# Kernel optimization log

Hardware: AMD Instinct MI355X
Metric: run time of the kernel (lower is better)

The kernel has to match this reference:

```python
import jax, jax.numpy as jnp
import numpy as np

N = 50000      # nodes
E = 640000     # edges
HID = 64       # hid_dim (per-head channels C)
HEADS = 4
D = HID * HEADS  # 256, conv output dim (concat=True)
LN_EPS = 1e-5


def setup_inputs() -> dict:
    key = jax.random.key(0)
    ks = jax.random.split(key, 10)
    def w(k, shape, scale=0.05):
        return jax.random.normal(k, shape, dtype=jnp.float32) * scale
    x = jax.random.normal(ks[0], (N, HID), dtype=jnp.float32)
    edge_index = jax.random.randint(ks[1], (2, E), 0, N)
    return {
        'x': x,
        'edge_index': edge_index,
        'Wq': w(ks[2], (D, HID)), 'bq': jnp.zeros((D,), jnp.float32),
        'Wk': w(ks[3], (D, HID)), 'bk': jnp.zeros((D,), jnp.float32),
        'Wv': w(ks[4], (D, HID)), 'bv': jnp.zeros((D,), jnp.float32),
        'Wskip': w(ks[5], (D, HID)), 'bskip': jnp.zeros((D,), jnp.float32),
        'Wbeta': w(ks[6], (1, 3 * D)),
        'ln_g': jnp.ones((D,), jnp.float32), 'ln_b': jnp.zeros((D,), jnp.float32),
        'Wproj': w(ks[7], (HID, D)), 'bproj': jnp.zeros((HID,), jnp.float32),
    }


def _layer(x, edge_index, Wq, bq, Wk, bk, Wv, bv, Wskip, bskip, Wbeta, ln_g, ln_b, Wproj, bproj):
    src, dst = edge_index[0], edge_index[1]  # message flows src -> dst
    # q/k/v projections, [N, H, C]
    q = (x @ Wq.T + bq).reshape(N, HEADS, HID)
    k = (x @ Wk.T + bk).reshape(N, HEADS, HID)
    v = (x @ Wv.T + bv).reshape(N, HEADS, HID)
    # edge-wise attention logits: [E, H]
    alpha = jnp.einsum('ehc,ehc->eh', q[dst], k[src]) / jnp.sqrt(jnp.float32(HID))
    # per-destination-node softmax (segment softmax)
    m = jax.ops.segment_max(alpha, dst, num_segments=N)          # [N, H]
    ex = jnp.exp(alpha - m[dst])                                 # [E, H]
    s = jax.ops.segment_sum(ex, dst, num_segments=N)             # [N, H]
    attn = ex / (s[dst] + 1e-16)                                 # [E, H]
    # weighted scatter-aggregate of values -> [N, H*C]
    msg = (v[src] * attn[..., None]).reshape(E, D)
    out = jax.ops.segment_sum(msg, dst, num_segments=N)          # [N, D]
    # beta gated skip (TransformerConv beta=True, root_weight=True)
    x_r = x @ Wskip.T + bskip                                    # [N, D]
    beta = jax.nn.sigmoid(jnp.concatenate([out, x_r, out - x_r], axis=-1) @ Wbeta.T)  # [N, 1]
    h = beta * x_r + (1.0 - beta) * out
    # LayerNorm over last dim
    mu = jnp.mean(h, axis=-1, keepdims=True)
    var = jnp.var(h, axis=-1, keepdims=True)
    h = (h - mu) * jax.lax.rsqrt(var + LN_EPS) * ln_g + ln_b
    # projection + residual + ReLU (dropout = identity in eval)
    h = h @ Wproj.T + bproj
    return jax.nn.relu(h + x)


def reference(x, edge_index, Wq, bq, Wk, bk, Wv, bv, Wskip, bskip, Wbeta, ln_g, ln_b, Wproj, bproj):
    return _layer(x, edge_index, Wq, bq, Wk, bk, Wv, bv, Wskip, bskip, Wbeta, ln_g, ln_b, Wproj, bproj)
```

## Files before the change

### kernel.cpp

```cpp
#include <hip/hip_runtime.h>
#include <stdint.h>

#define NND 50000
#define NED 640000

typedef unsigned short u16;
typedef unsigned int u32;
typedef __attribute__((ext_vector_type(8))) short short8;
typedef __attribute__((ext_vector_type(4))) float f32x4;
typedef __attribute__((ext_vector_type(2))) float fx2;

__device__ __forceinline__ float bf2f(u16 u) {
    union { u32 i; float f; } x; x.i = ((u32)u) << 16; return x.f;
}
__device__ __forceinline__ u16 f2bf(float f) {
    union { u32 i; float f; } x; x.f = f;
    u32 u = x.i;
    return (u16)((u + 0x7fffu + ((u >> 16) & 1u)) >> 16);
}
__device__ __forceinline__ float bflo(u32 w) {
    union { u32 i; float f; } x; x.i = w << 16; return x.f;
}
__device__ __forceinline__ float bfhi(u32 w) {
    union { u32 i; float f; } x; x.i = w & 0xffff0000u; return x.f;
}
__device__ __forceinline__ u32 pk2(float lo, float hi) {
    return (u32)f2bf(lo) | ((u32)f2bf(hi) << 16);
}
__device__ __forceinline__ u32 pk_fp8_4(u32 w0, u32 w1) {
    u32 p = __builtin_amdgcn_cvt_pk_fp8_f32(bflo(w0), bfhi(w0), 0, false);
    p = __builtin_amdgcn_cvt_pk_fp8_f32(bflo(w1), bfhi(w1), p, true);
    return p;
}
__device__ __forceinline__ void dec8v(u32 a, u32 b, fx2* f) {
    f[0] = __builtin_amdgcn_cvt_pk_f32_fp8(a, false);
    f[1] = __builtin_amdgcn_cvt_pk_f32_fp8(a, true);
    f[2] = __builtin_amdgcn_cvt_pk_f32_fp8(b, false);
    f[3] = __builtin_amdgcn_cvt_pk_f32_fp8(b, true);
}

__global__ void k_wt(const float* __restrict__ Wq, const float* __restrict__ Wk,
                     const float* __restrict__ Wv, const float* __restrict__ Ws,
                     const float* __restrict__ Wp,
                     const float* __restrict__ bq, const float* __restrict__ bk,
                     const float* __restrict__ bv, const float* __restrict__ bs,
                     u16* __restrict__ wb, float* __restrict__ bias_c,
                     u16* __restrict__ wpA) {
    int idx = blockIdx.x * 256 + threadIdx.x;
    if (idx < 65536) {
        int j = idx & 7;
        int lane = (idx >> 3) & 63;
        int q = (idx >> 9) & 1;
        int dt = idx >> 10;
        int dim = dt * 16 + (lane & 15);
        int k = q * 32 + ((lane >> 4) & 3) * 8 + j;
        int mat = dim >> 8, r = dim & 255;
        const float* W = (mat == 0) ? Wq : (mat == 1) ? Wk : (mat == 2) ? Wv : Ws;
        float v = W[r * 64 + k] * ((mat == 0) ? 0.125f : 1.0f);
        wb[idx] = f2bf(v);
    } else if (idx < 65536 + 1024) {
        int dim = idx - 65536;
        int mat = dim >> 8, r = dim & 255;
        const float* B = (mat == 0) ? bq : (mat == 1) ? bk : (mat == 2) ? bv : bs;
        bias_c[dim] = B[r] * ((mat == 0) ? 0.125f : 1.0f);
    } else if (idx < 65536 + 1024 + 16384) {
        int w = idx - 66560;
        int j = w & 7;
        int lane = (w >> 3) & 63;
        int kc = (w >> 9) & 7;
        int mt = w >> 12;
        int dim = mt * 16 + (lane & 15);
        int k = kc * 32 + ((lane >> 4) & 3) * 8 + j;
        wpA[w] = f2bf(Wp[dim * 256 + k]);
    }
}

#define CNT_BLKS 2500
#define PPAD 1040
__global__ __launch_bounds__(256) void k_fillproj(
    const int* __restrict__ esrc, const int* __restrict__ edst,
    int* __restrict__ deg, int* __restrict__ csr,
    const float* __restrict__ x, const u16* __restrict__ wb,
    const float* __restrict__ bias_c,
    uint2* __restrict__ q8, uint4* __restrict__ kv8, u16* __restrict__ xr16)
{
    __shared__ u16 hb[16 * PPAD];
    if (blockIdx.x < CNT_BLKS) {
        int e = blockIdx.x * 256 + threadIdx.x;
        if (e < NED) {
            int d = edst[e];
            int pos = atomicAdd(&deg[d], 1);
            if (pos < 64) csr[(d << 6) + pos] = esrc[e];
        }
        return;
    }
    const int t = threadIdx.x;
    const int wave = t >> 6, lane = t & 63;
    const int node0 = (blockIdx.x - CNT_BLKS) * 16;
    const int lr = lane & 15, quad = lane >> 4;

    int node = node0 + lr;
    if (node > NND - 1) node = NND - 1;
    short8 xf0, xf1;
    {
        const float* xp = x + (size_t)node * 64 + quad * 8;
        float4 a = *reinterpret_cast<const float4*>(xp);
        float4 b = *reinterpret_cast<const float4*>(xp + 4);
        float4 c = *reinterpret_cast<const float4*>(xp + 32);
        float4 d = *reinterpret_cast<const float4*>(xp + 36);
        xf0[0] = (short)f2bf(a.x); xf0[1] = (short)f2bf(a.y);
        xf0[2] = (short)f2bf(a.z); xf0[3] = (short)f2bf(a.w);
        xf0[4] = (short)f2bf(b.x); xf0[5] = (short)f2bf(b.y);
        xf0[6] = (short)f2bf(b.z); xf0[7] = (short)f2bf(b.w);
        xf1[0] = (short)f2bf(c.x); xf1[1] = (short)f2bf(c.y);
        xf1[2] = (short)f2bf(c.z); xf1[3] = (short)f2bf(c.w);
        xf1[4] = (short)f2bf(d.x); xf1[5] = (short)f2bf(d.y);
        xf1[6] = (short)f2bf(d.z); xf1[7] = (short)f2bf(d.w);
    }
    #pragma unroll 4
    for (int dtl = 0; dtl < 16; ++dtl) {
        int dt = wave * 16 + dtl;
        const u16* wp = wb + (size_t)(dt * 2) * 512 + lane * 8;
        short8 a0 = *reinterpret_cast<const short8*>(wp);
        short8 a1 = *reinterpret_cast<const short8*>(wp + 512);
        f32x4 bias = *reinterpret_cast<const f32x4*>(bias_c + dt * 16 + quad * 4);
        f32x4 acc = {0.f, 0.f, 0.f, 0.f};
        acc = __builtin_amdgcn_mfma_f32_16x16x32_bf16(a0, xf0, acc, 0, 0, 0);
        acc = __builtin_amdgcn_mfma_f32_16x16x32_bf16(a1, xf1, acc, 0, 0, 0);
        uint2 st;
        st.x = pk2(acc[0] + bias[0], acc[1] + bias[1]);
        st.y = pk2(acc[2] + bias[2], acc[3] + bias[3]);
        *reinterpret_cast<uint2*>(&hb[lr * PPAD + dt * 16 + quad * 4]) = st;
    }
    __syncthreads();
    #pragma unroll
    for (int it = 0; it < 2; ++it) {
        int idx = it * 256 + t;
        int nip = idx >> 5, g = idx & 31;
        int gnode = node0 + nip;
        if (gnode < NND) {
            const u16* hp = &hb[nip * PPAD];
            *reinterpret_cast<uint4*>(xr16 + (size_t)gnode * 256 + g * 8) =
                *reinterpret_cast<const uint4*>(hp + 768 + g * 8);
            uint4 qw = *reinterpret_cast<const uint4*>(hp + g * 8);
            uint2 qs;
            qs.x = pk_fp8_4(qw.x, qw.y);
            qs.y = pk_fp8_4(qw.z, qw.w);
            q8[(size_t)gnode * 32 + g] = qs;
            uint4 kw = *reinterpret_cast<const uint4*>(hp + 256 + g * 8);
            uint4 vw = *reinterpret_cast<const uint4*>(hp + 512 + g * 8);
            uint4 kvs;
            kvs.x = pk_fp8_4(kw.x, kw.y);
            kvs.y = pk_fp8_4(kw.z, kw.w);
            kvs.z = pk_fp8_4(vw.x, vw.y);
            kvs.w = pk_fp8_4(vw.z, vw.w);
            kv8[(size_t)gnode * 32 + g] = kvs;
        }
    }
}

#define PS 264
__global__ __launch_bounds__(256) void k_attnepi(
    const int* __restrict__ deg, const int* __restrict__ csr,
    const uint2* __restrict__ q8, const uint4* __restrict__ kv8,
    const u16* __restrict__ xr16, const float* __restrict__ x,
    const float* __restrict__ Wbeta, const float* __restrict__ ln_g,
    const float* __restrict__ ln_b, const u16* __restrict__ wpA,
    const float* __restrict__ bproj, float* __restrict__ y)
{
    __shared__ u16 hn[16 * PS];
    const int t = threadIdx.x;
    const int wave = t >> 6, lane = t & 63;
    const int l32 = lane & 31, half = lane >> 5;
    const int lr = lane & 15, grp = lane >> 4;
    const int base = blockIdx.x * 16;

    for (int nt = 0; nt < 4; ++nt) {
        int lid = wave * 4 + nt;
        int node = base + lid;
        if (node >= NND) break;
        uint2 qv = q8[(size_t)node * 32 + l32];
        fx2 q[4];
        dec8v(qv.x, qv.y, q);
        int dg = __builtin_amdgcn_readfirstlane(deg[node]);
        if (dg > 64) dg = 64;
        int r0 = node << 6;
        int r1 = r0 + dg;
        float s = 0.f;
        fx2 acc0 = {0.f, 0.f}, acc1 = {0.f, 0.f}, acc2 = {0.f, 0.f}, acc3 = {0.f, 0.f};
        int i = r0;
        for (; i + 8 <= r1; i += 8) {
            int c0 = csr[i + 0], c1 = csr[i + 1], c2 = csr[i + 2], c3 = csr[i + 3];
            int c4 = csr[i + 4], c5 = csr[i + 5], c6 = csr[i + 6], c7 = csr[i + 7];
            int e0 = half ? c4 : c0;
            int e1 = half ? c5 : c1;
            int e2 = half ? c6 : c2;
            int e3 = half ? c7 : c3;
            uint4 kv0 = kv8[(size_t)e0 * 32 + l32];
            uint4 kv1 = kv8[(size_t)e1 * 32 + l32];
            uint4 kv2 = kv8[(size_t)e2 * 32 + l32];
            uint4 kv3 = kv8[(size_t)e3 * 32 + l32];
            fx2 k0[4], k1[4], k2[4], k3[4];
            dec8v(kv0.x, kv0.y, k0); dec8v(kv1.x, kv1.y, k1);
            dec8v(kv2.x, kv2.y, k2); dec8v(kv3.x, kv3.y, k3);
            fx2 t0 = q[0]*k0[0] + q[1]*k0[1] + q[2]*k0[2] + q[3]*k0[3];
            fx2 t1 = q[0]*k1[0] + q[1]*k1[1] + q[2]*k1[2] + q[3]*k1[3];
            fx2 t2 = q[0]*k2[0] + q[1]*k2[1] + q[2]*k2[2] + q[3]*k2[3];
            fx2 t3 = q[0]*k3[0] + q[1]*k3[1] + q[2]*k3[2] + q[3]*k3[3];
            float pa = t0.x + t0.y, pb = t1.x + t1.y, pc = t2.x + t2.y, pd = t3.x + t3.y;
            pa += __shfl_xor(pa, 1); pa += __shfl_xor(pa, 2); pa += __shfl_xor(pa, 4);
            pb += __shfl_xor(pb, 1); pb += __shfl_xor(pb, 2); pb += __shfl_xor(pb, 4);
            pc += __shfl_xor(pc, 1); pc += __shfl_xor(pc, 2); pc += __shfl_xor(pc, 4);
            pd += __shfl_xor(pd, 1); pd += __shfl_xor(pd, 2); pd += __shfl_xor(pd, 4);
            float ea = __expf(pa), eb = __expf(pb), ec = __expf(pc), ed = __expf(pd);
            s += (ea + eb) + (ec + ed);
            fx2 ev0 = {ea, ea}, ev1 = {eb, eb}, ev2 = {ec, ec}, ev3 = {ed, ed};
            fx2 v0[4], v1[4], v2[4], v3[4];
            dec8v(kv0.z, kv0.w, v0); dec8v(kv1.z, kv1.w, v1);
            dec8v(kv2.z, kv2.w, v2); dec8v(kv3.z, kv3.w, v3);
            acc0 = acc0 + ev0*v0[0] + ev1*v1[0] + ev2*v2[0] + ev3*v3[0];
            acc1 = acc1 + ev0*v0[1] + ev1*v1[1] + ev2*v2[1] + ev3*v3[1];
            acc2 = acc2 + ev0*v0[2] + ev1*v1[2] + ev2*v2[2] + ev3*v3[2];
            acc3 = acc3 + ev0*v0[3] + ev1*v1[3] + ev2*v2[3] + ev3*v3[3];
        }
        for (; i + 4 <= r1; i += 4) {
            int c0 = csr[i + 0], c1 = csr[i + 1], c2 = csr[i + 2], c3 = csr[i + 3];
            int e0 = half ? c2 : c0;
            int e1 = half ? c3 : c1;
            uint4 kv0 = kv8[(size_t)e0 * 32 + l32];
            uint4 kv1 = kv8[(size_t)e1 * 32 + l32];
            fx2 k0[4], k1[4];
            dec8v(kv0.x, kv0.y, k0); dec8v(kv1.x, kv1.y, k1);
            fx2 t0 = q[0]*k0[0] + q[1]*k0[1] + q[2]*k0[2] + q[3]*k0[3];
            fx2 t1 = q[0]*k1[0] + q[1]*k1[1] + q[2]*k1[2] + q[3]*k1[3];
            float pa = t0.x + t0.y, pb = t1.x + t1.y;
            pa += __shfl_xor(pa, 1); pa += __shfl_xor(pa, 2); pa += __shfl_xor(pa, 4);
            pb += __shfl_xor(pb, 1); pb += __shfl_xor(pb, 2); pb += __shfl_xor(pb, 4);
            float ea = __expf(pa), eb = __expf(pb);
            s += ea + eb;
            fx2 ev0 = {ea, ea}, ev1 = {eb, eb};
            fx2 v0[4], v1[4];
            dec8v(kv0.z, kv0.w, v0); dec8v(kv1.z, kv1.w, v1);
            acc0 = acc0 + ev0*v0[0] + ev1*v1[0];
            acc1 = acc1 + ev0*v0[1] + ev1*v1[1];
            acc2 = acc2 + ev0*v0[2] + ev1*v1[2];
            acc3 = acc3 + ev0*v0[3] + ev1*v1[3];
        }
        for (; i < r1; i += 2) {
            int ii = i + half;
            bool valid = ii < r1;
            if (ii > r1 - 1) ii = r1 - 1;
            int e0 = csr[ii];
            uint4 kv0 = kv8[(size_t)e0 * 32 + l32];
            fx2 k0[4];
            dec8v(kv0.x, kv0.y, k0);
            fx2 t0 = q[0]*k0[0] + q[1]*k0[1] + q[2]*k0[2] + q[3]*k0[3];
            float pa = t0.x + t0.y;
            pa += __shfl_xor(pa, 1); pa += __shfl_xor(pa, 2); pa += __shfl_xor(pa, 4);
            float ea = valid ? __expf(pa) : 0.f;
            s += ea;
            fx2 ev0 = {ea, ea};
            fx2 v0[4];
            dec8v(kv0.z, kv0.w, v0);
            acc0 = acc0 + ev0*v0[0];
            acc1 = acc1 + ev0*v0[1];
            acc2 = acc2 + ev0*v0[2];
            acc3 = acc3 + ev0*v0[3];
        }
        float a0 = acc0.x, a1 = acc0.y, a2 = acc1.x, a3 = acc1.y;
        float a4 = acc2.x, a5 = acc2.y, a6 = acc3.x, a7 = acc3.y;
        s  += __shfl_xor(s, 32);
        a0 += __shfl_xor(a0, 32); a1 += __shfl_xor(a1, 32);
        a2 += __shfl_xor(a2, 32); a3 += __shfl_xor(a3, 32);
        a4 += __shfl_xor(a4, 32); a5 += __shfl_xor(a5, 32);
        a6 += __shfl_xor(a6, 32); a7 += __shfl_xor(a7, 32);
        float inv = 1.0f / (s + 1e-16f);
        if (half == 0) {
            uint4 st;
            st.x = pk2(a0 * inv, a1 * inv);
            st.y = pk2(a2 * inv, a3 * inv);
            st.z = pk2(a4 * inv, a5 * inv);
            st.w = pk2(a6 * inv, a7 * inv);
            *reinterpret_cast<uint4*>(&hn[lid * PS + l32 * 8]) = st;
        }
    }
    __syncthreads();

    {
        const float4* wb4 = reinterpret_cast<const float4*>(Wbeta);
        const float4* g44 = reinterpret_cast<const float4*>(ln_g);
        const float4* b44 = reinterpret_cast<const float4*>(ln_b);
        float wo[16], wx[16], wd[16], gg[16], bb[16];
        #pragma unroll
        for (int j = 0; j < 4; ++j) {
            float4 a = wb4[lr * 4 + j];
            float4 b = wb4[64 + lr * 4 + j];
            float4 c = wb4[128 + lr * 4 + j];
            float4 g = g44[lr * 4 + j];
            float4 bl = b44[lr * 4 + j];
            wo[j*4+0]=a.x; wo[j*4+1]=a.y; wo[j*4+2]=a.z; wo[j*4+3]=a.w;
            wx[j*4+0]=b.x; wx[j*4+1]=b.y; wx[j*4+2]=b.z; wx[j*4+3]=b.w;
            wd[j*4+0]=c.x; wd[j*4+1]=c.y; wd[j*4+2]=c.z; wd[j*4+3]=c.w;
            gg[j*4+0]=g.x; gg[j*4+1]=g.y; gg[j*4+2]=g.z; gg[j*4+3]=g.w;
            bb[j*4+0]=bl.x; bb[j*4+1]=bl.y; bb[j*4+2]=bl.z; bb[j*4+3]=bl.w;
        }
        int lid = wave * 4 + grp;
        int node = base + lid;
        if (node < NND) {
            uint4 u0 = *reinterpret_cast<const uint4*>(&hn[lid * PS + lr * 16]);
            uint4 u1 = *reinterpret_cast<const uint4*>(&hn[lid * PS + lr * 16 + 8]);
            const uint4* xp = reinterpret_cast<const uint4*>(xr16 + (size_t)node * 256 + lr * 16);
            uint4 v0 = xp[0], v1 = xp[1];
            float o[16], r[16];
            o[0]=bflo(u0.x); o[1]=bfhi(u0.x); o[2]=bflo(u0.y); o[3]=bfhi(u0.y);
            o[4]=bflo(u0.z); o[5]=bfhi(u0.z); o[6]=bflo(u0.w); o[7]=bfhi(u0.w);
            o[8]=bflo(u1.x); o[9]=bfhi(u1.x); o[10]=bflo(u1.y); o[11]=bfhi(u1.y);
            o[12]=bflo(u1.z); o[13]=bfhi(u1.z); o[14]=bflo(u1.w); o[15]=bfhi(u1.w);
            r[0]=bflo(v0.x); r[1]=bfhi(v0.x); r[2]=bflo(v0.y); r[3]=bfhi(v0.y);
            r[4]=bflo(v0.z); r[5]=bfhi(v0.z); r[6]=bflo(v0.w); r[7]=bfhi(v0.w);
            r[8]=bflo(v1.x); r[9]=bfhi(v1.x); r[10]=bflo(v1.y); r[11]=bfhi(v1.y);
            r[12]=bflo(v1.z); r[13]=bfhi(v1.z); r[14]=bflo(v1.w); r[15]=bfhi(v1.w);
            float part = 0.f;
            #pragma unroll
            for (int cc = 0; cc < 16; ++cc)
                part = fmaf(wo[cc], o[cc], fmaf(wx[cc], r[cc], fmaf(wd[cc], o[cc]-r[cc], part)));
            part += __shfl_xor(part, 1); part += __shfl_xor(part, 2);
            part += __shfl_xor(part, 4); part += __shfl_xor(part, 8);
            float beta = 1.0f / (1.0f + __expf(-part));
            float h[16];
            float sh = 0.f, sq = 0.f;
            #pragma unroll
            for (int cc = 0; cc < 16; ++cc) {
                h[cc] = beta * r[cc] + (1.f - beta) * o[cc];
                sh += h[cc];
                sq = fmaf(h[cc], h[cc], sq);
            }
            sh += __shfl_xor(sh, 1); sh += __shfl_xor(sh, 2);
            sh += __shfl_xor(sh, 4); sh += __shfl_xor(sh, 8);
            sq += __shfl_xor(sq, 1); sq += __shfl_xor(sq, 2);
            sq += __shfl_xor(sq, 4); sq += __shfl_xor(sq, 8);
            float mu = sh * (1.0f / 256.0f);
            float var = sq * (1.0f / 256.0f) - mu * mu;
            float ri = rsqrtf(var + 1e-5f);
            u32 pw[8];
            #pragma unroll
            for (int pp = 0; pp < 8; ++pp) {
                float z0 = (h[pp*2+0] - mu) * ri * gg[pp*2+0] + bb[pp*2+0];
                float z1 = (h[pp*2+1] - mu) * ri * gg[pp*2+1] + bb[pp*2+1];
                pw[pp] = pk2(z0, z1);
            }
            uint4 s0, s1;
            s0.x = pw[0]; s0.y = pw[1]; s0.z = pw[2]; s0.w = pw[3];
            s1.x = pw[4]; s1.y = pw[5]; s1.z = pw[6]; s1.w = pw[7];
            *reinterpret_cast<uint4*>(&hn[lid * PS + lr * 16]) = s0;
            *reinterpret_cast<uint4*>(&hn[lid * PS + lr * 16 + 8]) = s1;
        }
    }
    __syncthreads();

    {
        const int mt = wave;
        f32x4 acc = {0.f, 0.f, 0.f, 0.f};
        #pragma unroll
        for (int kc = 0; kc < 8; ++kc) {
            short8 a = *reinterpret_cast<const short8*>(wpA + ((size_t)(mt * 8 + kc) * 64 + lane) * 8);
            short8 b = *reinterpret_cast<const short8*>(&hn[lr * PS + kc * 32 + grp * 8]);
            acc = __builtin_amdgcn_mfma_f32_16x16x32_bf16(a, b, acc, 0, 0, 0);
        }
        int node = base + lr;
        if (node < NND) {
            int d0 = mt * 16 + grp * 4;
            float4 bp4 = *reinterpret_cast<const float4*>(bproj + d0);
            float4 xv = *reinterpret_cast<const float4*>(x + (size_t)node * 64 + d0);
            float4 rr;
            rr.x = fmaxf(acc[0] + bp4.x + xv.x, 0.f);
            rr.y = fmaxf(acc[1] + bp4.y + xv.y, 0.f);
            rr.z = fmaxf(acc[2] + bp4.z + xv.z, 0.f);
            rr.w = fmaxf(acc[3] + bp4.w + xv.w, 0.f);
            *reinterpret_cast<float4*>(y + (size_t)node * 64 + d0) = rr;
        }
    }
}

extern "C" void kernel_launch(void* const* d_in, const int* in_sizes, int n_in,
                              void* d_out, int out_size, void* d_ws, size_t ws_size,
                              hipStream_t stream) {
    const float* x     = (const float*)d_in[0];
    const int*   eidx  = (const int*)d_in[1];
    const float* Wq    = (const float*)d_in[2];
    const float* bq    = (const float*)d_in[3];
    const float* Wk    = (const float*)d_in[4];
    const float* bk    = (const float*)d_in[5];
    const float* Wv    = (const float*)d_in[6];
    const float* bv    = (const float*)d_in[7];
    const float* Wsk   = (const float*)d_in[8];
    const float* bsk   = (const float*)d_in[9];
    const float* Wbeta = (const float*)d_in[10];
    const float* lng   = (const float*)d_in[11];
    const float* lnb   = (const float*)d_in[12];
    const float* Wp    = (const float*)d_in[13];
    const float* bp    = (const float*)d_in[14];
    float* y = (float*)d_out;

    char* ws = (char*)d_ws;
    size_t off = 0;
    auto alloc = [&](size_t b) { size_t o = off; off += (b + 255) & ~(size_t)255; return o; };
    uint2* q8   = (uint2*)(ws + alloc((size_t)NND * 256));
    uint4* kv8  = (uint4*)(ws + alloc((size_t)NND * 512));
    u16*  xr16  = (u16*)(ws + alloc((size_t)NND * 512));
    int* deg    = (int*)(ws + alloc((size_t)NND * 4));
    int* csr    = (int*)(ws + alloc((size_t)NND * 64 * 4));
    u16* wb     = (u16*)(ws + alloc((size_t)65536 * 2));
    float* bias_c = (float*)(ws + alloc((size_t)1024 * 4));
    u16* wpA    = (u16*)(ws + alloc((size_t)16384 * 2));

    hipMemsetAsync(deg, 0, (size_t)NND * 4, stream);
    k_wt      <<<324, 256, 0, stream>>>(Wq, Wk, Wv, Wsk, Wp, bq, bk, bv, bsk,
                                        wb, bias_c, wpA);
    k_fillproj<<<CNT_BLKS + (NND + 15) / 16, 256, 0, stream>>>(
                 eidx, eidx + NED, deg, csr, x, wb, bias_c, q8, kv8, xr16);
    k_attnepi <<<(NND + 15) / 16, 256, 0, stream>>>(deg, csr, q8, kv8, xr16, x,
                                                    Wbeta, lng, lnb, wpA, bp, y);
}
```

Before: 238.4 us.

## Remap attention gather to two nodes per wave with prefetched neighbor loop

Restructures the edge-aggregation phase so each half-wave handles one node, and each 16-lane group processes one edge with 16-byte-per-lane loads. CSR indices and q are preloaded into registers and shared through shuffles. A software-pipelined loop prefetches the next edge pair's K/V while processing the current one. The separate deg memset is folded into the weight-prep kernel, and the node bounds checks are removed because NND divides evenly by 16. Risks include divergence when the two nodes sharing a wave have very different degrees, and higher register use.

Measured after the change: 225.9 us. 5.2% less time.

```diff
diff --git a/kernel.cpp b/kernel.cpp
--- a/kernel.cpp
+++ b/kernel.cpp
@@ -45,7 +45,7 @@
                      const float* __restrict__ bq, const float* __restrict__ bk,
                      const float* __restrict__ bv, const float* __restrict__ bs,
                      u16* __restrict__ wb, float* __restrict__ bias_c,
-                     u16* __restrict__ wpA) {
+                     u16* __restrict__ wpA, int* __restrict__ deg) {
     int idx = blockIdx.x * 256 + threadIdx.x;
     if (idx < 65536) {
         int j = idx & 7;
@@ -72,6 +72,8 @@
         int dim = mt * 16 + (lane & 15);
         int k = kc * 32 + ((lane >> 4) & 3) * 8 + j;
         wpA[w] = f2bf(Wp[dim * 256 + k]);
+    } else if (idx < 65536 + 1024 + 16384 + NND) {
+        deg[idx - 82944] = 0;
     }
 }
 
@@ -160,6 +162,7 @@
 }
 
 #define PS 264
+#define NPB 16
 __global__ __launch_bounds__(256) void k_attnepi(
     const int* __restrict__ deg, const int* __restrict__ csr,
     const uint2* __restrict__ q8, const uint4* __restrict__ kv8,
@@ -168,120 +171,111 @@
     const float* __restrict__ ln_b, const u16* __restrict__ wpA,
     const float* __restrict__ bproj, float* __restrict__ y)
 {
-    __shared__ u16 hn[16 * PS];
+    __shared__ u16 hn[NPB * PS];
     const int t = threadIdx.x;
-    const int wave = t >> 6, lane = t & 63;
-    const int l32 = lane & 31, half = lane >> 5;
+    const int wave = __builtin_amdgcn_readfirstlane(t >> 6);
+    const int lane = t & 63;
+    const int sub = lane & 31, h = lane >> 5;
+    const int es = (sub >> 4) & 1, dl = sub & 15;
     const int lr = lane & 15, grp = lane >> 4;
-    const int base = blockIdx.x * 16;
-
-    for (int nt = 0; nt < 4; ++nt) {
-        int lid = wave * 4 + nt;
-        int node = base + lid;
-        if (node >= NND) break;
-        uint2 qv = q8[(size_t)node * 32 + l32];
-        fx2 q[4];
-        dec8v(qv.x, qv.y, q);
-        int dg = __builtin_amdgcn_readfirstlane(deg[node]);
-        if (dg > 64) dg = 64;
-        int r0 = node << 6;
-        int r1 = r0 + dg;
+    const int base = blockIdx.x * NPB;
+
+    int dg_[2], ia_[2], ib_[2];
+    uint4 qv_[2];
+    #pragma unroll
+    for (int p = 0; p < 2; ++p) {
+        int node = base + wave * 4 + 2 * p + h;
+        int dgv = deg[node];
+        dg_[p] = dgv > 64 ? 64 : dgv;
+        ia_[p] = csr[(node << 6) + sub];
+        ib_[p] = csr[(node << 6) + 32 + sub];
+        qv_[p] = *reinterpret_cast<const uint4*>(
+            reinterpret_cast<const char*>(q8) + (size_t)node * 256 + dl * 16);
+    }
+    const uint4* kvb = kv8 + (dl << 1);
+    #pragma unroll
+    for (int p = 0; p < 2; ++p) {
+        const int dg = dg_[p];
+        const int ia = ia_[p], ib = ib_[p];
+        fx2 q[8];
+        dec8v(qv_[p].x, qv_[p].y, q);
+        dec8v(qv_[p].z, qv_[p].w, q + 4);
+        int dgo = __shfl_xor(dg, 32);
+        int mdg = __builtin_amdgcn_readfirstlane(dg > dgo ? dg : dgo);
+
         float s = 0.f;
-        fx2 acc0 = {0.f, 0.f}, acc1 = {0.f, 0.f}, acc2 = {0.f, 0.f}, acc3 = {0.f, 0.f};
-        int i = r0;
-        for (; i + 8 <= r1; i += 8) {
-            int c0 = csr[i + 0], c1 = csr[i + 1], c2 = csr[i + 2], c3 = csr[i + 3];
-            int c4 = csr[i + 4], c5 = csr[i + 5], c6 = csr[i + 6], c7 = csr[i + 7];
-            int e0 = half ? c4 : c0;
-            int e1 = half ? c5 : c1;
-            int e2 = half ? c6 : c2;
-            int e3 = half ? c7 : c3;
-            uint4 kv0 = kv8[(size_t)e0 * 32 + l32];
-            uint4 kv1 = kv8[(size_t)e1 * 32 + l32];
-            uint4 kv2 = kv8[(size_t)e2 * 32 + l32];
-            uint4 kv3 = kv8[(size_t)e3 * 32 + l32];
-            fx2 k0[4], k1[4], k2[4], k3[4];
-            dec8v(kv0.x, kv0.y, k0); dec8v(kv1.x, kv1.y, k1);
-            dec8v(kv2.x, kv2.y, k2); dec8v(kv3.x, kv3.y, k3);
-            fx2 t0 = q[0]*k0[0] + q[1]*k0[1] + q[2]*k0[2] + q[3]*k0[3];
-            fx2 t1 = q[0]*k1[0] + q[1]*k1[1] + q[2]*k1[2] + q[3]*k1[3];
-            fx2 t2 = q[0]*k2[0] + q[1]*k2[1] + q[2]*k2[2] + q[3]*k2[3];
-            fx2 t3 = q[0]*k3[0] + q[1]*k3[1] + q[2]*k3[2] + q[3]*k3[3];
-            float pa = t0.x + t0.y, pb = t1.x + t1.y, pc = t2.x + t2.y, pd = t3.x + t3.y;
-            pa += __shfl_xor(pa, 1); pa += __shfl_xor(pa, 2); pa += __shfl_xor(pa, 4);
-            pb += __shfl_xor(pb, 1); pb += __shfl_xor(pb, 2); pb += __shfl_xor(pb, 4);
-            pc += __shfl_xor(pc, 1); pc += __shfl_xor(pc, 2); pc += __shfl_xor(pc, 4);
-            pd += __shfl_xor(pd, 1); pd += __shfl_xor(pd, 2); pd += __shfl_xor(pd, 4);
-            float ea = __expf(pa), eb = __expf(pb), ec = __expf(pc), ed = __expf(pd);
-            s += (ea + eb) + (ec + ed);
-            fx2 ev0 = {ea, ea}, ev1 = {eb, eb}, ev2 = {ec, ec}, ev3 = {ed, ed};
-            fx2 v0[4], v1[4], v2[4], v3[4];
-            dec8v(kv0.z, kv0.w, v0); dec8v(kv1.z, kv1.w, v1);
-            dec8v(kv2.z, kv2.w, v2); dec8v(kv3.z, kv3.w, v3);
-            acc0 = acc0 + ev0*v0[0] + ev1*v1[0] + ev2*v2[0] + ev3*v3[0];
-            acc1 = acc1 + ev0*v0[1] + ev1*v1[1] + ev2*v2[1] + ev3*v3[1];
-            acc2 = acc2 + ev0*v0[2] + ev1*v1[2] + ev2*v2[2] + ev3*v3[2];
-            acc3 = acc3 + ev0*v0[3] + ev1*v1[3] + ev2*v2[3] + ev3*v3[3];
-        }
-        for (; i + 4 <= r1; i += 4) {
-            int c0 = csr[i + 0], c1 = csr[i + 1], c2 = csr[i + 2], c3 = csr[i + 3];
-            int e0 = half ? c2 : c0;
-            int e1 = half ? c3 : c1;
-            uint4 kv0 = kv8[(size_t)e0 * 32 + l32];
-            uint4 kv1 = kv8[(size_t)e1 * 32 + l32];
-            fx2 k0[4], k1[4];
-            dec8v(kv0.x, kv0.y, k0); dec8v(kv1.x, kv1.y, k1);
-            fx2 t0 = q[0]*k0[0] + q[1]*k0[1] + q[2]*k0[2] + q[3]*k0[3];
-            fx2 t1 = q[0]*k1[0] + q[1]*k1[1] + q[2]*k1[2] + q[3]*k1[3];
-            float pa = t0.x + t0.y, pb = t1.x + t1.y;
-            pa += __shfl_xor(pa, 1); pa += __shfl_xor(pa, 2); pa += __shfl_xor(pa, 4);
-            pb += __shfl_xor(pb, 1); pb += __shfl_xor(pb, 2); pb += __shfl_xor(pb, 4);
-            float ea = __expf(pa), eb = __expf(pb);
-            s += ea + eb;
-            fx2 ev0 = {ea, ea}, ev1 = {eb, eb};
-            fx2 v0[4], v1[4];
-            dec8v(kv0.z, kv0.w, v0); dec8v(kv1.z, kv1.w, v1);
-            acc0 = acc0 + ev0*v0[0] + ev1*v1[0];
-            acc1 = acc1 + ev0*v0[1] + ev1*v1[1];
-            acc2 = acc2 + ev0*v0[2] + ev1*v1[2];
-            acc3 = acc3 + ev0*v0[3] + ev1*v1[3];
-        }
-        for (; i < r1; i += 2) {
-            int ii = i + half;
-            bool valid = ii < r1;
-            if (ii > r1 - 1) ii = r1 - 1;
-            int e0 = csr[ii];
-            uint4 kv0 = kv8[(size_t)e0 * 32 + l32];
-            fx2 k0[4];
-            dec8v(kv0.x, kv0.y, k0);
-            fx2 t0 = q[0]*k0[0] + q[1]*k0[1] + q[2]*k0[2] + q[3]*k0[3];
-            float pa = t0.x + t0.y;
-            pa += __shfl_xor(pa, 1); pa += __shfl_xor(pa, 2); pa += __shfl_xor(pa, 4);
-            float ea = valid ? __expf(pa) : 0.f;
+        fx2 acc[8];
+        #pragma unroll
+        for (int r = 0; r < 8; ++r) acc[r] = fx2{0.f, 0.f};
+
+        auto fetch = [&](int i, uint4& c0, uint4& c1) {
+            int j = i + es;
+            int lsrc = (h << 5) | (j & 31);
+            int r0 = __shfl(ia, lsrc);
+            int r1 = __shfl(ib, lsrc);
+            int e = (j & 32) ? r1 : r0;
+            if ((u32)e >= NND) e = 0;
+            const uint4* kp = kvb + ((size_t)e << 5);
+            c0 = kp[0];
+            c1 = kp[1];
+        };
+        auto process = [&](int i, uint4 c0, uint4 c1) {
+            int j = i + es;
+            fx2 kk[8];
+            dec8v(c0.x, c0.y, kk);
+            dec8v(c1.x, c1.y, kk + 4);
+            fx2 d0 = q[0] * kk[0] + q[1] * kk[1];
+            fx2 d1 = q[2] * kk[2] + q[3] * kk[3];
+            fx2 d2 = q[4] * kk[4] + q[5] * kk[5];
+            fx2 d3 = q[6] * kk[6] + q[7] * kk[7];
+            fx2 dd = (d0 + d1) + (d2 + d3);
+            float pa = dd.x + dd.y;
+            pa += __shfl_xor(pa, 1);
+            pa += __shfl_xor(pa, 2);
+            float ea = __expf(pa);
+            ea = (j < dg) ? ea : 0.f;
             s += ea;
-            fx2 ev0 = {ea, ea};
-            fx2 v0[4];
-            dec8v(kv0.z, kv0.w, v0);
-            acc0 = acc0 + ev0*v0[0];
-            acc1 = acc1 + ev0*v0[1];
-            acc2 = acc2 + ev0*v0[2];
-            acc3 = acc3 + ev0*v0[3];
-        }
-        float a0 = acc0.x, a1 = acc0.y, a2 = acc1.x, a3 = acc1.y;
-        float a4 = acc2.x, a5 = acc2.y, a6 = acc3.x, a7 = acc3.y;
-        s  += __shfl_xor(s, 32);
-        a0 += __shfl_xor(a0, 32); a1 += __shfl_xor(a1, 32);
-        a2 += __shfl_xor(a2, 32); a3 += __shfl_xor(a3, 32);
-        a4 += __shfl_xor(a4, 32); a5 += __shfl_xor(a5, 32);
-        a6 += __shfl_xor(a6, 32); a7 += __shfl_xor(a7, 32);
+            fx2 ev = {ea, ea};
+            fx2 vv[8];
+            dec8v(c0.z, c0.w, vv);
+            dec8v(c1.z, c1.w, vv + 4);
+            acc[0] += ev * vv[0]; acc[1] += ev * vv[1];
+            acc[2] += ev * vv[2]; acc[3] += ev * vv[3];
+            acc[4] += ev * vv[4]; acc[5] += ev * vv[5];
+            acc[6] += ev * vv[6]; acc[7] += ev * vv[7];
+        };
+
+        if (mdg > 0) {
+            uint4 c0, c1, n0, n1;
+            fetch(0, c0, c1);
+            int i = 0;
+            for (; i + 2 < mdg; i += 2) {
+                fetch(i + 2, n0, n1);
+                process(i, c0, c1);
+                c0 = n0; c1 = n1;
+            }
+            process(i, c0, c1);
+        }
+        #pragma unroll
+        for (int r = 0; r < 8; ++r) {
+            acc[r].x += __shfl_xor(acc[r].x, 16);
+            acc[r].y += __shfl_xor(acc[r].y, 16);
+        }
+        s += __shfl_xor(s, 16);
         float inv = 1.0f / (s + 1e-16f);
-        if (half == 0) {
-            uint4 st;
-            st.x = pk2(a0 * inv, a1 * inv);
-            st.y = pk2(a2 * inv, a3 * inv);
-            st.z = pk2(a4 * inv, a5 * inv);
-            st.w = pk2(a6 * inv, a7 * inv);
-            *reinterpret_cast<uint4*>(&hn[lid * PS + l32 * 8]) = st;
+        if (es == 0) {
+            int lid = wave * 4 + 2 * p + h;
+            uint4 s0, s1;
+            s0.x = pk2(acc[0].x * inv, acc[0].y * inv);
+            s0.y = pk2(acc[1].x * inv, acc[1].y * inv);
+            s0.z = pk2(acc[2].x * inv, acc[2].y * inv);
+            s0.w = pk2(acc[3].x * inv, acc[3].y * inv);
+            s1.x = pk2(acc[4].x * inv, acc[4].y * inv);
+            s1.y = pk2(acc[5].x * inv, acc[5].y * inv);
+            s1.z = pk2(acc[6].x * inv, acc[6].y * inv);
+            s1.w = pk2(acc[7].x * inv, acc[7].y * inv);
+            *reinterpret_cast<uint4*>(&hn[lid * PS + dl * 16]) = s0;
+            *reinterpret_cast<uint4*>(&hn[lid * PS + dl * 16 + 8]) = s1;
         }
     }
     __syncthreads();
@@ -306,7 +300,7 @@
         }
         int lid = wave * 4 + grp;
         int node = base + lid;
-        if (node < NND) {
+        {
             uint4 u0 = *reinterpret_cast<const uint4*>(&hn[lid * PS + lr * 16]);
             uint4 u1 = *reinterpret_cast<const uint4*>(&hn[lid * PS + lr * 16 + 8]);
             const uint4* xp = reinterpret_cast<const uint4*>(xr16 + (size_t)node * 256 + lr * 16);
@@ -327,13 +321,13 @@
             part += __shfl_xor(part, 1); part += __shfl_xor(part, 2);
             part += __shfl_xor(part, 4); part += __shfl_xor(part, 8);
             float beta = 1.0f / (1.0f + __expf(-part));
-            float h[16];
+            float hh[16];
             float sh = 0.f, sq = 0.f;
             #pragma unroll
             for (int cc = 0; cc < 16; ++cc) {
-                h[cc] = beta * r[cc] + (1.f - beta) * o[cc];
-                sh += h[cc];
-                sq = fmaf(h[cc], h[cc], sq);
+                hh[cc] = beta * r[cc] + (1.f - beta) * o[cc];
+                sh += hh[cc];
+                sq = fmaf(hh[cc], hh[cc], sq);
             }
             sh += __shfl_xor(sh, 1); sh += __shfl_xor(sh, 2);
             sh += __shfl_xor(sh, 4); sh += __shfl_xor(sh, 8);
@@ -345,8 +339,8 @@
             u32 pw[8];
             #pragma unroll
             for (int pp = 0; pp < 8; ++pp) {
-                float z0 = (h[pp*2+0] - mu) * ri * gg[pp*2+0] + bb[pp*2+0];
-                float z1 = (h[pp*2+1] - mu) * ri * gg[pp*2+1] + bb[pp*2+1];
+                float z0 = (hh[pp*2+0] - mu) * ri * gg[pp*2+0] + bb[pp*2+0];
+                float z1 = (hh[pp*2+1] - mu) * ri * gg[pp*2+1] + bb[pp*2+1];
                 pw[pp] = pk2(z0, z1);
             }
             uint4 s0, s1;
@@ -368,7 +362,7 @@
             acc = __builtin_amdgcn_mfma_f32_16x16x32_bf16(a, b, acc, 0, 0, 0);
         }
         int node = base + lr;
-        if (node < NND) {
+        {
             int d0 = mt * 16 + grp * 4;
             float4 bp4 = *reinterpret_cast<const float4*>(bproj + d0);
             float4 xv = *reinterpret_cast<const float4*>(x + (size_t)node * 64 + d0);
@@ -414,11 +408,10 @@
     float* bias_c = (float*)(ws + alloc((size_t)1024 * 4));
     u16* wpA    = (u16*)(ws + alloc((size_t)16384 * 2));
 
-    hipMemsetAsync(deg, 0, (size_t)NND * 4, stream);
-    k_wt      <<<324, 256, 0, stream>>>(Wq, Wk, Wv, Wsk, Wp, bq, bk, bv, bsk,
-                                        wb, bias_c, wpA);
+    k_wt      <<<520, 256, 0, stream>>>(Wq, Wk, Wv, Wsk, Wp, bq, bk, bv, bsk,
+                                        wb, bias_c, wpA, deg);
     k_fillproj<<<CNT_BLKS + (NND + 15) / 16, 256, 0, stream>>>(
                  eidx, eidx + NED, deg, csr, x, wb, bias_c, q8, kv8, xr16);
-    k_attnepi <<<(NND + 15) / 16, 256, 0, stream>>>(deg, csr, q8, kv8, xr16, x,
-                                                    Wbeta, lng, lnb, wpA, bp, y);
-}
+    k_attnepi <<<(NND + NPB - 1) / NPB, 256, 0, stream>>>(deg, csr, q8, kv8, xr16, x,
+                                                          Wbeta, lng, lnb, wpA, bp, y);
+}
```
